# Optimization experiments

Measured on AMD Instinct MI355X. Metric: run time of the kernel, lower is better.

## Reference

```python
import jax, jax.numpy as jnp
import numpy as np

B, T, C, H = 2, 2048, 1024, 16
D = C // H  # head_dim = 64

def setup_inputs() -> dict:
    key = jax.random.key(0)
    k1, k2, k3 = jax.random.split(key, 3)
    x = jax.random.normal(k1, (B, T, C), dtype=jnp.float32)
    W_qkv = jax.random.normal(k2, (C, 3 * C), dtype=jnp.float32) * (C ** -0.5)
    b_qkv = jnp.zeros((3 * C,), dtype=jnp.float32)
    W_proj = jax.random.normal(k3, (C, C), dtype=jnp.float32) * (C ** -0.5)
    b_proj = jnp.zeros((C,), dtype=jnp.float32)
    return {"x": x, "W_qkv": W_qkv, "b_qkv": b_qkv, "W_proj": W_proj, "b_proj": b_proj}

def reference(x, W_qkv, b_qkv, W_proj, b_proj):
    # qkv projection: [B,T,3C]
    qkv = jnp.einsum('btc,cf->btf', x, W_qkv) + b_qkv
    q, k, v = jnp.split(qkv, 3, axis=-1)
    # split heads -> [B,H,T,D]
    q = q.reshape(B, T, H, D).transpose(0, 2, 1, 3)
    k = k.reshape(B, T, H, D).transpose(0, 2, 1, 3)
    v = v.reshape(B, T, H, D).transpose(0, 2, 1, 3)
    scale = 1.0 / jnp.sqrt(jnp.float32(D))
    att = jnp.einsum('bhqd,bhkd->bhqk', q, k) * scale  # [B,H,T,T]
    causal = jnp.tril(jnp.ones((T, T), dtype=bool))
    att = jnp.where(causal[None, None, :, :], att, jnp.float32(-jnp.inf))
    att = jax.nn.softmax(att, axis=-1)
    y = jnp.einsum('bhqk,bhkd->bhqd', att, v)  # [B,H,T,D]
    y = y.transpose(0, 2, 1, 3).reshape(B, T, C)
    return jnp.einsum('btc,cf->btf', y, W_proj) + b_proj
```

## Files before the change

### kernel.cpp

```cpp
#include <hip/hip_runtime.h>
#include <hip/hip_bf16.h>

#define Bq 2
#define Tq 2048
#define Cq 1024
#define Hq 16
#define Dq 64
#define Mq (Bq * Tq)

typedef __bf16 bf16x8 __attribute__((ext_vector_type(8)));
typedef float f32x4 __attribute__((ext_vector_type(4)));
typedef unsigned uint4v __attribute__((ext_vector_type(4)));
typedef unsigned short u16;

static __device__ __forceinline__ u16 f2bf(float f) {
  union { float f; unsigned u; } v; v.f = f;
  return (u16)((v.u + 0x7fffu + ((v.u >> 16) & 1u)) >> 16);
}

static __device__ __forceinline__ unsigned cvt_pk_bf16(float a, float b) {
  unsigned r;
  asm("v_cvt_pk_bf16_f32 %0, %1, %2" : "=v"(r) : "v"(a), "v"(b));
  return r;
}

static __device__ __forceinline__ f32x4 mfma16(bf16x8 a, bf16x8 b, f32x4 c) {
  return __builtin_amdgcn_mfma_f32_16x16x32_bf16(a, b, c, 0, 0, 0);
}

#define GLD16(g, l)                                                   \
  __builtin_amdgcn_global_load_lds(                                   \
      (const __attribute__((address_space(1))) unsigned int*)(g),     \
      (__attribute__((address_space(3))) unsigned int*)(l), 16, 0, 0)

static __device__ __forceinline__ int sperm(int k) {
  return (k & 0x23) | ((k & 0x0C) << 1) | ((k & 0x10) >> 2);
}

__global__ __launch_bounds__(256) void convert_x(const float* __restrict__ x,
                                                 u16* __restrict__ xb) {
  int i = (blockIdx.x * 256 + threadIdx.x) * 8;
  float4 a = *(const float4*)(x + i);
  float4 b = *(const float4*)(x + i + 4);
  u16 tmp[8];
  tmp[0] = f2bf(a.x); tmp[1] = f2bf(a.y); tmp[2] = f2bf(a.z); tmp[3] = f2bf(a.w);
  tmp[4] = f2bf(b.x); tmp[5] = f2bf(b.y); tmp[6] = f2bf(b.z); tmp[7] = f2bf(b.w);
  *(uint4*)(xb + i) = *(const uint4*)tmp;
}

__global__ __launch_bounds__(256) void transpose_w(const float* __restrict__ W,
                                                   u16* __restrict__ Wt,
                                                   int K, int N) {
  __shared__ __align__(16) u16 Ts[64][72];
  const int k0 = blockIdx.x * 64, n0 = blockIdx.y * 64;
  const int t = threadIdx.x;
  const int r = t >> 2, c0 = (t & 3) * 16;
  const float* src = W + (size_t)(k0 + r) * N + n0 + c0;
  u16 v16[16];
#pragma unroll
  for (int i = 0; i < 4; i++) {
    float4 f = *(const float4*)(src + 4 * i);
    v16[4 * i + 0] = f2bf(f.x); v16[4 * i + 1] = f2bf(f.y);
    v16[4 * i + 2] = f2bf(f.z); v16[4 * i + 3] = f2bf(f.w);
  }
#pragma unroll
  for (int j = 0; j < 16; j++) Ts[c0 + j][r] = v16[j];
  __syncthreads();
  u16* dst = Wt + (size_t)(n0 + r) * K + k0 + c0;
  *(uint4*)dst = *(const uint4*)&Ts[r][c0];
  *(uint4*)(dst + 8) = *(const uint4*)&Ts[r][c0 + 8];
}

__global__ __launch_bounds__(256) void transpose_v(const u16* __restrict__ vw,
                                                   u16* __restrict__ vts) {
  __shared__ __align__(16) u16 Ts[64][72];
  const int tile = blockIdx.x, bh = blockIdx.y;
  const size_t base = (size_t)bh * Tq * Dq;
  const int t = threadIdx.x;
  const int rv = t >> 2, c0 = (t & 3) * 16;
  const u16* src = vw + base + (size_t)(tile * 64 + rv) * Dq + c0;
  union { uint4 q[2]; u16 s[16]; } vu;
  vu.q[0] = *(const uint4*)src;
  vu.q[1] = *(const uint4*)(src + 8);
  const int sc = sperm(rv);
#pragma unroll
  for (int j = 0; j < 16; j++) Ts[c0 + j][sc] = vu.s[j];
  __syncthreads();
  u16* dst = vts + base + (size_t)rv * Tq + tile * 64 + c0;
  *(uint4*)dst = *(const uint4*)&Ts[rv][c0];
  *(uint4*)(dst + 8) = *(const uint4*)&Ts[rv][c0 + 8];
}

__global__ __launch_bounds__(256) void qkv_gemm(
    const u16* __restrict__ A, const u16* __restrict__ Bt,
    const float* __restrict__ bias,
    u16* __restrict__ qw, u16* __restrict__ kw, u16* __restrict__ vw) {
  const int K = 1024;
  __shared__ __align__(16) u16 As[128][32];
  __shared__ __align__(16) u16 Bs[128][32];
  const int m0 = blockIdx.x * 128, n0 = blockIdx.y * 128;
  const int t = threadIdx.x, lane = t & 63, w = t >> 6;
  const int wm = (w >> 1) * 64, wn = (w & 1) * 64;
  const int l15 = lane & 15, l4 = lane >> 4;
  const int lr = lane >> 2, lc = (lane & 3) * 8;
  f32x4 acc[4][4] = {};
  const u16* ga = A + (size_t)(m0 + w * 16 + lr) * K + lc;
  const u16* gb = Bt + (size_t)(n0 + w * 16 + lr) * K + lc;

  for (int kk = 0; kk < K; kk += 32) {
    __syncthreads();
    GLD16(ga + kk, &As[w * 16][0]);
    GLD16(ga + (size_t)64 * K + kk, &As[64 + w * 16][0]);
    GLD16(gb + kk, &Bs[w * 16][0]);
    GLD16(gb + (size_t)64 * K + kk, &Bs[64 + w * 16][0]);
    __syncthreads();
    bf16x8 af[4], bfr[4];
#pragma unroll
    for (int i = 0; i < 4; i++) {
      af[i] = *(const bf16x8*)&As[wm + i * 16 + l15][l4 * 8];
      bfr[i] = *(const bf16x8*)&Bs[wn + i * 16 + l15][l4 * 8];
    }
#pragma unroll
    for (int mi = 0; mi < 4; mi++)
#pragma unroll
      for (int ni = 0; ni < 4; ni++)
        acc[mi][ni] = mfma16(af[mi], bfr[ni], acc[mi][ni]);
  }
  const int which = n0 >> 10;
  u16* dst = (which == 0) ? qw : ((which == 1) ? kw : vw);
  const float qsc = (which == 0) ? 0.18033688011112042f : 1.0f;
#pragma unroll
  for (int mi = 0; mi < 4; mi++) {
#pragma unroll
    for (int ni = 0; ni < 4; ni++) {
#pragma unroll
      for (int r = 0; r < 4; r++) {
        int row = m0 + wm + mi * 16 + l4 * 4 + r;
        int col = n0 + wn + ni * 16 + l15;
        float val = (acc[mi][ni][r] + bias[col]) * qsc;
        int c = col & 1023;
        int h = c >> 6, d = c & 63;
        int b = row >> 11, tt = row & 2047;
        dst[(size_t)((b * Hq + h) * Tq + tt) * Dq + d] = f2bf(val);
      }
    }
  }
}

__global__ __launch_bounds__(256, 2) void attn(
    const u16* __restrict__ qw, const u16* __restrict__ kw,
    const u16* __restrict__ vts, u16* __restrict__ yw) {
  const int bh = blockIdx.x;
  const int qy = blockIdx.y;
  const int qb = (qy < 8) ? (15 - qy) : (qy - 8);
  __shared__ __align__(16) u16 Ks[2][64][64];
  __shared__ __align__(16) u16 Vt[2][64][64];
  const int t = threadIdx.x, lane = t & 63, w = t >> 6;
  const int l15 = lane & 15, l4 = lane >> 4;
  const size_t base = (size_t)bh * Tq * Dq;
  const int qs0 = qb * 128 + w * 32;

  bf16x8 qf[2][2];
  {
    const u16* qp = qw + base + (size_t)(qs0 + l15) * Dq + l4 * 8;
    qf[0][0] = *(const bf16x8*)qp;
    qf[0][1] = *(const bf16x8*)(qp + 32);
    qf[1][0] = *(const bf16x8*)(qp + 16 * Dq);
    qf[1][1] = *(const bf16x8*)(qp + 16 * Dq + 32);
  }

  const int r0 = w * 8 + (lane >> 3);
  const int c0 = ((lane & 7) ^ (r0 & 7)) * 8;
  const u16* kbase = kw + base;
  const u16* vbase = vts + base;

#define STAGE(kv_, b_)                                                      \
  do {                                                                      \
    GLD16(kbase + (size_t)((kv_)*64 + r0) * Dq + c0, &Ks[b_][w * 8][0]);    \
    GLD16(kbase + (size_t)((kv_)*64 + 32 + r0) * Dq + c0,                   \
          &Ks[b_][32 + w * 8][0]);                                          \
    GLD16(vbase + (size_t)r0 * Tq + (kv_)*64 + c0, &Vt[b_][w * 8][0]);      \
    GLD16(vbase + (size_t)(32 + r0) * Tq + (kv_)*64 + c0,                   \
          &Vt[b_][32 + w * 8][0]);                                          \
  } while (0)

  float m[2] = {-1e30f, -1e30f}, lsum[2] = {0.f, 0.f};
  f32x4 accO[2][4] = {};
  const int kvmax = 2 * qb + 1;

  STAGE(0, 0);
  __syncthreads();

  for (int kv = 0; kv <= kvmax; kv++) {
    const int cur = kv & 1;
    if (kv < kvmax) STAGE(kv + 1, cur ^ 1);

    if (kv * 64 <= qs0 + 31) {
      f32x4 sc[2][4];
      __builtin_amdgcn_s_setprio(1);
#pragma unroll
      for (int ct = 0; ct < 4; ct++) {
        const int kr = ct * 16 + l15, e = l15 & 7;
        bf16x8 kf0 = *(const bf16x8*)&Ks[cur][kr][8 * (l4 ^ e)];
        bf16x8 kf1 = *(const bf16x8*)&Ks[cur][kr][8 * ((4 + l4) ^ e)];
        f32x4 z0 = {};
        z0 = mfma16(kf0, qf[0][0], z0); z0 = mfma16(kf1, qf[0][1], z0);
        sc[0][ct] = z0;
        f32x4 z1 = {};
        z1 = mfma16(kf0, qf[1][0], z1); z1 = mfma16(kf1, qf[1][1], z1);
        sc[1][ct] = z1;
      }
      __builtin_amdgcn_s_setprio(0);

      if (kv * 64 + 63 > qs0) {
#pragma unroll
        for (int s = 0; s < 2; s++) {
          const int q = qs0 + s * 16 + l15;
#pragma unroll
          for (int ct = 0; ct < 4; ct++)
#pragma unroll
            for (int r = 0; r < 4; r++) {
              int k = kv * 64 + ct * 16 + l4 * 4 + r;
              if (k > q) sc[s][ct][r] = -1e30f;
            }
        }
      }

      bf16x8 pa[2][2];
#pragma unroll
      for (int s = 0; s < 2; s++) {
        float pmax = sc[s][0][0];
#pragma unroll
        for (int ct = 0; ct < 4; ct++)
#pragma unroll
          for (int r = 0; r < 4; r++) pmax = fmaxf(pmax, sc[s][ct][r]);
        pmax = fmaxf(pmax, __shfl_xor(pmax, 16));
        pmax = fmaxf(pmax, __shfl_xor(pmax, 32));

        if (__any(pmax > m[s] + 8.f)) {
          float mn = fmaxf(m[s], pmax);
          float corr = exp2f(m[s] - mn);
          m[s] = mn;
          lsum[s] *= corr;
#pragma unroll
          for (int r = 0; r < 4; r++) {
            float cb = __shfl(corr, (lane >> 4) * 20 + r);
#pragma unroll
            for (int dt = 0; dt < 4; dt++) accO[s][dt][r] *= cb;
          }
        }

        float psum = 0.f;
#pragma unroll
        for (int ct = 0; ct < 4; ct++)
#pragma unroll
          for (int r = 0; r < 4; r++) {
            float p = exp2f(sc[s][ct][r] - m[s]);
            sc[s][ct][r] = p;
            psum += p;
          }
        psum += __shfl_xor(psum, 16);
        psum += __shfl_xor(psum, 32);
        lsum[s] += psum;

#pragma unroll
        for (int h = 0; h < 2; h++) {
          uint4v pu;
          pu[0] = cvt_pk_bf16(sc[s][2 * h][0], sc[s][2 * h][1]);
          pu[1] = cvt_pk_bf16(sc[s][2 * h][2], sc[s][2 * h][3]);
          pu[2] = cvt_pk_bf16(sc[s][2 * h + 1][0], sc[s][2 * h + 1][1]);
          pu[3] = cvt_pk_bf16(sc[s][2 * h + 1][2], sc[s][2 * h + 1][3]);
          pa[s][h] = __builtin_bit_cast(bf16x8, pu);
        }
      }

      __builtin_amdgcn_s_setprio(1);
#pragma unroll
      for (int dt = 0; dt < 4; dt++) {
        const int Rv = dt * 16 + l15, e = l15 & 7;
        bf16x8 vf0 = *(const bf16x8*)&Vt[cur][Rv][8 * (l4 ^ e)];
        bf16x8 vf1 = *(const bf16x8*)&Vt[cur][Rv][8 * ((4 + l4) ^ e)];
        accO[0][dt] = mfma16(pa[0][0], vf0, accO[0][dt]);
        accO[0][dt] = mfma16(pa[0][1], vf1, accO[0][dt]);
        accO[1][dt] = mfma16(pa[1][0], vf0, accO[1][dt]);
        accO[1][dt] = mfma16(pa[1][1], vf1, accO[1][dt]);
      }
      __builtin_amdgcn_s_setprio(0);
    }
    __syncthreads();
  }
#undef STAGE

  const int b = bh >> 4, hd = bh & 15;
#pragma unroll
  for (int s = 0; s < 2; s++) {
    float inv = 1.0f / lsum[s];
#pragma unroll
    for (int r = 0; r < 4; r++) {
      float ib = __shfl(inv, (lane >> 4) * 20 + r);
      int tt = qs0 + s * 16 + l4 * 4 + r;
      size_t rowbase = ((size_t)(b * Tq + tt)) * Cq + hd * 64;
#pragma unroll
      for (int dt = 0; dt < 4; dt++)
        yw[rowbase + dt * 16 + l15] = f2bf(accO[s][dt][r] * ib);
    }
  }
}

__global__ __launch_bounds__(256) void proj_gemm(
    const u16* __restrict__ A, const u16* __restrict__ Bt,
    const float* __restrict__ bias, float* __restrict__ out) {
  const int K = 1024, N = 1024;
  __shared__ __align__(16) u16 As[128][32];
  __shared__ __align__(16) u16 Bs[128][32];
  const int m0 = blockIdx.x * 128, n0 = blockIdx.y * 128;
  const int t = threadIdx.x, lane = t & 63, w = t >> 6;
  const int wm = (w >> 1) * 64, wn = (w & 1) * 64;
  const int l15 = lane & 15, l4 = lane >> 4;
  const int lr = lane >> 2, lc = (lane & 3) * 8;
  f32x4 acc[4][4] = {};
  const u16* ga = A + (size_t)(m0 + w * 16 + lr) * K + lc;
  const u16* gb = Bt + (size_t)(n0 + w * 16 + lr) * K + lc;

  for (int kk = 0; kk < K; kk += 32) {
    __syncthreads();
    GLD16(ga + kk, &As[w * 16][0]);
    GLD16(ga + (size_t)64 * K + kk, &As[64 + w * 16][0]);
    GLD16(gb + kk, &Bs[w * 16][0]);
    GLD16(gb + (size_t)64 * K + kk, &Bs[64 + w * 16][0]);
    __syncthreads();
    bf16x8 af[4], bfr[4];
#pragma unroll
    for (int i = 0; i < 4; i++) {
      af[i] = *(const bf16x8*)&As[wm + i * 16 + l15][l4 * 8];
      bfr[i] = *(const bf16x8*)&Bs[wn + i * 16 + l15][l4 * 8];
    }
#pragma unroll
    for (int mi = 0; mi < 4; mi++)
#pragma unroll
      for (int ni = 0; ni < 4; ni++)
        acc[mi][ni] = mfma16(af[mi], bfr[ni], acc[mi][ni]);
  }
#pragma unroll
  for (int mi = 0; mi < 4; mi++) {
#pragma unroll
    for (int ni = 0; ni < 4; ni++) {
#pragma unroll
      for (int r = 0; r < 4; r++) {
        int row = m0 + wm + mi * 16 + l4 * 4 + r;
        int col = n0 + wn + ni * 16 + l15;
        out[(size_t)row * N + col] = acc[mi][ni][r] + bias[col];
      }
    }
  }
}

extern "C" void kernel_launch(void* const* d_in, const int* in_sizes, int n_in,
                              void* d_out, int out_size, void* d_ws, size_t ws_size,
                              hipStream_t stream) {
  const float* x = (const float*)d_in[0];
  const float* W_qkv = (const float*)d_in[1];
  const float* b_qkv = (const float*)d_in[2];
  const float* W_proj = (const float*)d_in[3];
  const float* b_proj = (const float*)d_in[4];
  float* out = (float*)d_out;

  const size_t qkv_elems = (size_t)Bq * Hq * Tq * Dq;
  u16* qw = (u16*)d_ws;
  u16* kw = qw + qkv_elems;
  u16* vw = kw + qkv_elems;
  u16* xb = vw + qkv_elems;
  u16* wt = xb + (size_t)Mq * Cq;
  u16* vts = xb;
  u16* yw = vw;

  convert_x<<<dim3((Mq * Cq) / (256 * 8)), 256, 0, stream>>>(x, xb);
  transpose_w<<<dim3(Cq / 64, 3 * Cq / 64), 256, 0, stream>>>(W_qkv, wt, Cq, 3 * Cq);
  qkv_gemm<<<dim3(Mq / 128, 3 * Cq / 128), 256, 0, stream>>>(xb, wt, b_qkv, qw, kw, vw);
  transpose_v<<<dim3(Tq / 64, Bq * Hq), 256, 0, stream>>>(vw, vts);
  transpose_w<<<dim3(Cq / 64, Cq / 64), 256, 0, stream>>>(W_proj, wt, Cq, Cq);
  attn<<<dim3(Bq * Hq, Tq / 128), 256, 0, stream>>>(qw, kw, vts, yw);
  proj_gemm<<<dim3(Mq / 128, Cq / 128), 256, 0, stream>>>(yw, wt, b_proj, out);
}
```

Baseline: 219.3 us.

## Widen attention KV tile to 128 with fine-grained causal skipping

The attention kernel now stages 128 keys and values per loop iteration instead of 64, which halves the number of barriers and double-buffer swaps per query block. On the diagonal tile it skips causally masked 16-key sub-tiles and 32-key PV chunks. The cross-lane row-sum reduction is deferred to the epilogue, and the row-max shuffles run only when a rescale is triggered. The cost is double the LDS footprint and more live score registers, which may reduce occupancy or cause spills.

```diff
diff --git a/kernel.cpp b/kernel.cpp
--- a/kernel.cpp
+++ b/kernel.cpp
@@ -153,8 +153,8 @@
   const int bh = blockIdx.x;
   const int qy = blockIdx.y;
   const int qb = (qy < 8) ? (15 - qy) : (qy - 8);
-  __shared__ __align__(16) u16 Ks[2][64][64];
-  __shared__ __align__(16) u16 Vt[2][64][64];
+  __shared__ __align__(16) u16 Ks[2][128][64];
+  __shared__ __align__(16) u16 Vt[2][64][128];
   const int t = threadIdx.x, lane = t & 63, w = t >> 6;
   const int l15 = lane & 15, l4 = lane >> 4;
   const size_t base = (size_t)bh * Tq * Dq;
@@ -169,38 +169,47 @@
     qf[1][1] = *(const bf16x8*)(qp + 16 * Dq + 32);
   }
 
-  const int r0 = w * 8 + (lane >> 3);
-  const int c0 = ((lane & 7) ^ (r0 & 7)) * 8;
+  const int kl_r = lane >> 3, kl_c = lane & 7;
+  const int vl_r = lane >> 4, vl_c = lane & 15;
+  const int vhb = vl_c >> 3, vgg = vl_c & 7;
   const u16* kbase = kw + base;
   const u16* vbase = vts + base;
 
-#define STAGE(kv_, b_)                                                      \
-  do {                                                                      \
-    GLD16(kbase + (size_t)((kv_)*64 + r0) * Dq + c0, &Ks[b_][w * 8][0]);    \
-    GLD16(kbase + (size_t)((kv_)*64 + 32 + r0) * Dq + c0,                   \
-          &Ks[b_][32 + w * 8][0]);                                          \
-    GLD16(vbase + (size_t)r0 * Tq + (kv_)*64 + c0, &Vt[b_][w * 8][0]);      \
-    GLD16(vbase + (size_t)(32 + r0) * Tq + (kv_)*64 + c0,                   \
-          &Vt[b_][32 + w * 8][0]);                                          \
+#define STAGE(kv_, b_)                                                       \
+  do {                                                                       \
+    _Pragma("unroll") for (int i = 0; i < 4; i++) {                          \
+      int r = i * 32 + w * 8 + kl_r;                                         \
+      GLD16(kbase + (size_t)((kv_)*128 + r) * Dq + ((kl_c ^ (r & 7)) * 8),   \
+            &Ks[b_][i * 32 + w * 8][0]);                                     \
+    }                                                                        \
+    _Pragma("unroll") for (int i = 0; i < 4; i++) {                          \
+      int r = i * 16 + w * 4 + vl_r;                                         \
+      GLD16(vbase + (size_t)r * Tq + (kv_)*128 + vhb * 64 +                  \
+                ((vgg ^ (r & 7)) * 8),                                       \
+            &Vt[b_][i * 16 + w * 4][0]);                                     \
+    }                                                                        \
   } while (0)
 
   float m[2] = {-1e30f, -1e30f}, lsum[2] = {0.f, 0.f};
   f32x4 accO[2][4] = {};
-  const int kvmax = 2 * qb + 1;
 
   STAGE(0, 0);
   __syncthreads();
 
-  for (int kv = 0; kv <= kvmax; kv++) {
+  for (int kv = 0; kv <= qb; kv++) {
     const int cur = kv & 1;
-    if (kv < kvmax) STAGE(kv + 1, cur ^ 1);
-
-    if (kv * 64 <= qs0 + 31) {
-      f32x4 sc[2][4];
-      __builtin_amdgcn_s_setprio(1);
-#pragma unroll
-      for (int ct = 0; ct < 4; ct++) {
-        const int kr = ct * 16 + l15, e = l15 & 7;
+    if (kv < qb) STAGE(kv + 1, cur ^ 1);
+
+    const int span = qs0 + 31 - kv * 128;
+    const int ctmax = (span >= 127) ? 8 : ((span >> 4) + 1);
+    const int hmax = (span >= 127) ? 4 : ((span >> 5) + 1);
+
+    f32x4 sc[2][8];
+    __builtin_amdgcn_s_setprio(1);
+#pragma unroll
+    for (int ct = 0; ct < 8; ct++) {
+      if (ct < ctmax) {
+        const int kr = ct * 16 + l15, e = kr & 7;
         bf16x8 kf0 = *(const bf16x8*)&Ks[cur][kr][8 * (l4 ^ e)];
         bf16x8 kf1 = *(const bf16x8*)&Ks[cur][kr][8 * ((4 + l4) ^ e)];
         f32x4 z0 = {};
@@ -210,83 +219,91 @@
         z1 = mfma16(kf0, qf[1][0], z1); z1 = mfma16(kf1, qf[1][1], z1);
         sc[1][ct] = z1;
       }
-      __builtin_amdgcn_s_setprio(0);
-
-      if (kv * 64 + 63 > qs0) {
-#pragma unroll
-        for (int s = 0; s < 2; s++) {
-          const int q = qs0 + s * 16 + l15;
-#pragma unroll
-          for (int ct = 0; ct < 4; ct++)
+    }
+    __builtin_amdgcn_s_setprio(0);
+
+    if (kv == qb) {
+#pragma unroll
+      for (int s = 0; s < 2; s++) {
+        const int q = qs0 + s * 16 + l15;
+#pragma unroll
+        for (int ct = 0; ct < 8; ct++) {
+          if (ct < ctmax) {
 #pragma unroll
             for (int r = 0; r < 4; r++) {
-              int k = kv * 64 + ct * 16 + l4 * 4 + r;
+              int k = kv * 128 + ct * 16 + l4 * 4 + r;
               if (k > q) sc[s][ct][r] = -1e30f;
             }
-        }
-      }
-
-      bf16x8 pa[2][2];
-#pragma unroll
-      for (int s = 0; s < 2; s++) {
-        float pmax = sc[s][0][0];
-#pragma unroll
-        for (int ct = 0; ct < 4; ct++)
+          }
+        }
+      }
+    }
+
+#pragma unroll
+    for (int s = 0; s < 2; s++) {
+      float pmax = -1e30f;
+#pragma unroll
+      for (int ct = 0; ct < 8; ct++)
+        if (ct < ctmax) {
 #pragma unroll
           for (int r = 0; r < 4; r++) pmax = fmaxf(pmax, sc[s][ct][r]);
+        }
+
+      if (__any(pmax > m[s] + 8.f)) {
         pmax = fmaxf(pmax, __shfl_xor(pmax, 16));
         pmax = fmaxf(pmax, __shfl_xor(pmax, 32));
-
-        if (__any(pmax > m[s] + 8.f)) {
-          float mn = fmaxf(m[s], pmax);
-          float corr = exp2f(m[s] - mn);
-          m[s] = mn;
-          lsum[s] *= corr;
-#pragma unroll
-          for (int r = 0; r < 4; r++) {
-            float cb = __shfl(corr, (lane >> 4) * 20 + r);
-#pragma unroll
-            for (int dt = 0; dt < 4; dt++) accO[s][dt][r] *= cb;
-          }
-        }
-
-        float psum = 0.f;
-#pragma unroll
-        for (int ct = 0; ct < 4; ct++)
+        float mn = fmaxf(m[s], pmax);
+        float corr = exp2f(m[s] - mn);
+        m[s] = mn;
+        lsum[s] *= corr;
+#pragma unroll
+        for (int r = 0; r < 4; r++) {
+          float cb = __shfl(corr, (lane >> 4) * 20 + r);
+#pragma unroll
+          for (int dt = 0; dt < 4; dt++) accO[s][dt][r] *= cb;
+        }
+      }
+
+      float psum = 0.f;
+#pragma unroll
+      for (int ct = 0; ct < 8; ct++)
+        if (ct < ctmax) {
 #pragma unroll
           for (int r = 0; r < 4; r++) {
             float p = exp2f(sc[s][ct][r] - m[s]);
             sc[s][ct][r] = p;
             psum += p;
           }
-        psum += __shfl_xor(psum, 16);
-        psum += __shfl_xor(psum, 32);
-        lsum[s] += psum;
-
-#pragma unroll
-        for (int h = 0; h < 2; h++) {
+        }
+      lsum[s] += psum;
+    }
+
+    __builtin_amdgcn_s_setprio(1);
+#pragma unroll
+    for (int h = 0; h < 4; h++) {
+      if (h < hmax) {
+        bf16x8 pa[2];
+#pragma unroll
+        for (int s = 0; s < 2; s++) {
           uint4v pu;
           pu[0] = cvt_pk_bf16(sc[s][2 * h][0], sc[s][2 * h][1]);
           pu[1] = cvt_pk_bf16(sc[s][2 * h][2], sc[s][2 * h][3]);
           pu[2] = cvt_pk_bf16(sc[s][2 * h + 1][0], sc[s][2 * h + 1][1]);
           pu[3] = cvt_pk_bf16(sc[s][2 * h + 1][2], sc[s][2 * h + 1][3]);
-          pa[s][h] = __builtin_bit_cast(bf16x8, pu);
-        }
-      }
-
-      __builtin_amdgcn_s_setprio(1);
-#pragma unroll
-      for (int dt = 0; dt < 4; dt++) {
-        const int Rv = dt * 16 + l15, e = l15 & 7;
-        bf16x8 vf0 = *(const bf16x8*)&Vt[cur][Rv][8 * (l4 ^ e)];
-        bf16x8 vf1 = *(const bf16x8*)&Vt[cur][Rv][8 * ((4 + l4) ^ e)];
-        accO[0][dt] = mfma16(pa[0][0], vf0, accO[0][dt]);
-        accO[0][dt] = mfma16(pa[0][1], vf1, accO[0][dt]);
-        accO[1][dt] = mfma16(pa[1][0], vf0, accO[1][dt]);
-        accO[1][dt] = mfma16(pa[1][1], vf1, accO[1][dt]);
-      }
-      __builtin_amdgcn_s_setprio(0);
-    }
+          pa[s] = __builtin_bit_cast(bf16x8, pu);
+        }
+#pragma unroll
+        for (int dt = 0; dt < 4; dt++) {
+          const int Rv = dt * 16 + l15, e = Rv & 7;
+          bf16x8 vf = *(const bf16x8*)&Vt[cur][Rv]
+              [(h >> 1) * 64 + 8 * ((((h & 1) * 4 + l4)) ^ e)];
+          accO[0][dt] = mfma16(pa[0], vf, accO[0][dt]);
+          accO[1][dt] = mfma16(pa[1], vf, accO[1][dt]);
+        }
+      }
+    }
+    __builtin_amdgcn_s_setprio(0);
+
     __syncthreads();
   }
 #undef STAGE
@@ -294,7 +311,10 @@
   const int b = bh >> 4, hd = bh & 15;
 #pragma unroll
   for (int s = 0; s < 2; s++) {
-    float inv = 1.0f / lsum[s];
+    float L = lsum[s];
+    L += __shfl_xor(L, 16);
+    L += __shfl_xor(L, 32);
+    float inv = 1.0f / L;
 #pragma unroll
     for (int r = 0; r < 4; r++) {
       float ib = __shfl(inv, (lane >> 4) * 20 + r);
```

Result: no change. 215.1 us (-1.9%).
